# Performance work log

Hardware: AMD Instinct MI355X
Metric: run time of the kernel (lower is better)

The kernel has to match this reference:

```python
import jax, jax.numpy as jnp
import numpy as np

B, L, Z, H = 8, 256, 16, 256


def setup_inputs() -> dict:
    key = jax.random.key(0)
    k1, k2, k3, k4 = jax.random.split(key, 4)
    start_logits = jax.random.normal(k1, (B, L, H), dtype=jnp.float32)
    end_logits = jax.random.normal(k2, (B, L, H), dtype=jnp.float32)
    cls_logits = jax.random.normal(k3, (B, Z, H), dtype=jnp.float32)
    # nn.init.normal_(std=0.1)
    weight_start_end = 0.1 * jax.random.normal(k4, (H, H, H), dtype=jnp.float32)
    return {
        "start_logits": start_logits,
        "end_logits": end_logits,
        "cls_logits": cls_logits,
        "weight_start_end": weight_start_end,
    }


def reference(start_logits, end_logits, cls_logits, weight_start_end):
    # start: [b,x,i], weight: [i,o,j], end: [b,y,j], cls: [b,z,o]
    # Stage 1a: contract i ->  [b,x,o,j]  (GEMM: (b*x, i) @ (i, o*j))
    sw = jnp.einsum('bxi,ioj->bxoj', start_logits, weight_start_end)
    # Stage 1b: contract j ->  [b,x,y,o]
    start_end = jnp.einsum('bxoj,byj->bxyo', sw, end_logits)
    # Stage 2: contract o ->  [b,x,y,z]
    span_logits = jnp.einsum('bxyo,bzo->bxyz', start_end, cls_logits)
    return span_logits
```

## Files before the change

### kernel.cpp

```cpp
#include <hip/hip_runtime.h>


typedef __attribute__((ext_vector_type(8))) short          bf16x8;
typedef __attribute__((ext_vector_type(8))) unsigned short u16x8;
typedef __attribute__((ext_vector_type(4))) unsigned short u16x4;
typedef __attribute__((ext_vector_type(4))) float          f32x4;

#define LDST 40

__device__ __forceinline__ unsigned short f2bf(float f) {
    unsigned u = __builtin_bit_cast(unsigned, f);
    u += 0x7fff + ((u >> 16) & 1);
    return (unsigned short)(u >> 16);
}

template<bool AB16, bool BB16, bool T2OUT>
__global__ __launch_bounds__(512, 4)
void gemm_trans(const void* __restrict__ Abv, const void* __restrict__ Bbv,
                unsigned short* __restrict__ Cb,
                int lda, int ldb, int ldc,
                long aBS, int aSh, long bBS, long cBS)
{
    __shared__ unsigned short As[2][128 * LDST];
    __shared__ unsigned short Bs[2][128 * LDST];

    const int tid  = threadIdx.x;
    const int bz   = blockIdx.z;
    const int row0 = blockIdx.y * 128;
    const int col0 = blockIdx.x * 128;

    const float*          Af = (const float*)Abv          + (long)(bz >> aSh) * aBS;
    const unsigned short* Ah = (const unsigned short*)Abv + (long)(bz >> aSh) * aBS;
    const float*          Bf = (const float*)Bbv          + (long)bz * bBS;
    const unsigned short* Bh = (const unsigned short*)Bbv + (long)bz * bBS;

    const int ar  = tid >> 2;
    const int akc = tid & 3;
    const int kp  = (tid & 15) * 2;
    const int ng  = (tid >> 4) * 4;

    const int wid = tid >> 6, lane = tid & 63;
    const int wm = wid >> 1, wn = wid & 1;
    const int lr = lane & 15, lg = lane >> 4;

    f32x4 acc[2][4] = {};

    float4 aPf[2][2]; u16x8 aPh[2];
    float4 bPf[2][2]; u16x4 bPh[2][2];

    auto LOAD = [&](int set, int k0) {
        if constexpr (!AB16) {
            const float* p = Af + (long)(row0 + ar) * lda + k0 + akc * 8;
            aPf[set][0] = *(const float4*)p;
            aPf[set][1] = *(const float4*)(p + 4);
        } else {
            aPh[set] = *(const u16x8*)(Ah + (long)(row0 + ar) * lda + k0 + akc * 8);
        }
        if constexpr (!BB16) {
            const float* q = Bf + (long)(k0 + kp) * ldb + col0 + ng;
            bPf[set][0] = *(const float4*)q;
            bPf[set][1] = *(const float4*)(q + ldb);
        } else {
            const unsigned short* q = Bh + (long)(k0 + kp) * ldb + col0 + ng;
            bPh[set][0] = *(const u16x4*)q;
            bPh[set][1] = *(const u16x4*)(q + ldb);
        }
    };

    auto WRITE = [&](int set, int buf) {
        u16x8 w;
        if constexpr (!AB16) {
            const float* v = (const float*)&aPf[set][0];
#pragma unroll
            for (int e = 0; e < 8; ++e) w[e] = f2bf(v[e]);
        } else {
            w = aPh[set];
        }
        *(u16x8*)(As[buf] + ar * LDST + akc * 8) = w;

#pragma unroll
        for (int e = 0; e < 4; ++e) {
            unsigned lo, hi;
            if constexpr (!BB16) {
                const float* v0 = (const float*)&bPf[set][0];
                const float* v1 = (const float*)&bPf[set][1];
                lo = f2bf(v0[e]); hi = f2bf(v1[e]);
            } else {
                lo = bPh[set][0][e]; hi = bPh[set][1][e];
            }
            *(unsigned*)(Bs[buf] + (ng + e) * LDST + kp) = lo | (hi << 16);
        }
    };

    auto COMPUTE = [&](int buf) {
        bf16x8 aF[2], bF[4];
#pragma unroll
        for (int fm = 0; fm < 2; ++fm)
            aF[fm] = *(const bf16x8*)&As[buf][(wm * 32 + fm * 16 + lr) * LDST + lg * 8];
#pragma unroll
        for (int fn = 0; fn < 4; ++fn)
            bF[fn] = *(const bf16x8*)&Bs[buf][(wn * 64 + fn * 16 + lr) * LDST + lg * 8];
#pragma unroll
        for (int fm = 0; fm < 2; ++fm)
#pragma unroll
            for (int fn = 0; fn < 4; ++fn)
                acc[fm][fn] = __builtin_amdgcn_mfma_f32_16x16x32_bf16(
                    aF[fm], bF[fn], acc[fm][fn], 0, 0, 0);
    };

    LOAD(0, 0);
    WRITE(0, 0);
    LOAD(1, 32);
#pragma unroll
    for (int s = 0; s < 8; ++s) {
        asm volatile("s_waitcnt lgkmcnt(0)" ::: "memory");
        __builtin_amdgcn_s_barrier();
        if (s < 6) LOAD(s & 1, (s + 2) * 32);
        COMPUTE(s & 1);
        if (s < 7) WRITE((s + 1) & 1, (s + 1) & 1);
    }

#pragma unroll
    for (int fm = 0; fm < 2; ++fm)
#pragma unroll
        for (int q = 0; q < 4; ++q) {
            const long row = row0 + wm * 32 + fm * 16 + lg * 4 + q;
#pragma unroll
            for (int fn = 0; fn < 4; ++fn) {
                const int col = col0 + wn * 64 + fn * 16 + lr;
                if constexpr (T2OUT) {
                    unsigned short* Cq = Cb + (long)(bz >> 4) * 1048576 + (bz & 15) * 256;
                    Cq[row * 4096 + col] = f2bf(acc[fm][fn][q]);
                } else {
                    unsigned short* Cq = Cb + (long)bz * cBS;
                    Cq[row * (long)ldc + col] = f2bf(acc[fm][fn][q]);
                }
            }
        }
}

__global__ __launch_bounds__(256)
void fused_out(const unsigned short* __restrict__ endbf,
               const unsigned short* __restrict__ T2,
               float* __restrict__ out)
{
    const int tid = threadIdx.x;
    const int b  = blockIdx.x >> 7;
    const int xp = blockIdx.x & 127;
    const int wid = tid >> 6, lane = tid & 63;
    const int lr = lane & 15, lg = lane >> 4;

    const unsigned short* Arow = endbf + (long)b * 65536;
    const unsigned short* B0 = T2 + ((long)(b * 256 + xp * 2) * 16 + lr) * 256;
    const unsigned short* B1 = B0 + 4096;

    f32x4 acc0[4] = {}, acc1[4] = {};
    u16x8 a[2][4], pb0[2], pb1[2];

    auto LOADF = [&](int set, int k0) {
#pragma unroll
        for (int fm = 0; fm < 4; ++fm)
            a[set][fm] = *(const u16x8*)(Arow + (long)(wid * 64 + fm * 16 + lr) * 256 + k0 + lg * 8);
        pb0[set] = *(const u16x8*)(B0 + k0 + lg * 8);
        pb1[set] = *(const u16x8*)(B1 + k0 + lg * 8);
    };

    LOADF(0, 0);
#pragma unroll
    for (int s = 0; s < 8; ++s) {
        if (s < 7) LOADF((s + 1) & 1, (s + 1) * 32);
        __builtin_amdgcn_s_setprio(1);
#pragma unroll
        for (int fm = 0; fm < 4; ++fm) {
            acc0[fm] = __builtin_amdgcn_mfma_f32_16x16x32_bf16(
                __builtin_bit_cast(bf16x8, a[s & 1][fm]),
                __builtin_bit_cast(bf16x8, pb0[s & 1]), acc0[fm], 0, 0, 0);
            acc1[fm] = __builtin_amdgcn_mfma_f32_16x16x32_bf16(
                __builtin_bit_cast(bf16x8, a[s & 1][fm]),
                __builtin_bit_cast(bf16x8, pb1[s & 1]), acc1[fm], 0, 0, 0);
        }
        __builtin_amdgcn_s_setprio(0);
    }

    float* op0 = out + (long)(b * 256 + xp * 2) * 4096;
    float* op1 = op0 + 4096;
#pragma unroll
    for (int fm = 0; fm < 4; ++fm)
#pragma unroll
        for (int q = 0; q < 4; ++q) {
            const int y = wid * 64 + fm * 16 + lg * 4 + q;
            op0[y * 16 + lr] = acc0[fm][q];
            op1[y * 16 + lr] = acc1[fm][q];
        }
}

__global__ __launch_bounds__(256)
void cvt_bf16(const float* __restrict__ endl, const float* __restrict__ start,
              unsigned short* __restrict__ endbf, unsigned short* __restrict__ startbf)
{
    const int which = blockIdx.x >> 8;
    const float* in = which ? start : endl;
    unsigned short* out = which ? startbf : endbf;
    const int i = ((blockIdx.x & 255) * 256 + threadIdx.x) * 8;
    float4 v0 = *(const float4*)(in + i);
    float4 v1 = *(const float4*)(in + i + 4);
    const float* v = (const float*)&v0;
    u16x8 w;
#pragma unroll
    for (int e = 0; e < 4; ++e) w[e] = f2bf(v[e]);
    const float* u = (const float*)&v1;
#pragma unroll
    for (int e = 0; e < 4; ++e) w[4 + e] = f2bf(u[e]);
    *(u16x8*)(out + i) = w;
}

extern "C" void kernel_launch(void* const* d_in, const int* in_sizes, int n_in,
                              void* d_out, int out_size, void* d_ws, size_t ws_size,
                              hipStream_t stream)
{
    const float* start = (const float*)d_in[0];
    const float* endl  = (const float*)d_in[1];
    const float* cls   = (const float*)d_in[2];
    const float* W     = (const float*)d_in[3];
    float* out = (float*)d_out;

    char* ws = (char*)d_ws;
    unsigned short* Wc      = (unsigned short*)ws;
    unsigned short* T2      = (unsigned short*)(ws + 16777216);
    unsigned short* endbf   = (unsigned short*)(ws + 33554432);
    unsigned short* startbf = (unsigned short*)(ws + 34603008);

    hipLaunchKernelGGL(cvt_bf16, dim3(512), dim3(256), 0, stream,
        endl, start, endbf, startbf);

    hipLaunchKernelGGL((gemm_trans<false, false, false>), dim3(2, 1, 256), dim3(512), 0, stream,
        (const void*)cls, (const void*)W, Wc, 256, 256, 65536, 0L, 0, 65536L, 256L);

    hipLaunchKernelGGL((gemm_trans<true, true, true>), dim3(2, 2, 128), dim3(512), 0, stream,
        (const void*)startbf, (const void*)Wc, T2, 256, 256, 4096, 65536L, 4, 65536L, 0L);

    hipLaunchKernelGGL(fused_out, dim3(1024), dim3(256), 0, stream, endbf, T2, out);
}
```

Baseline: 158.6 us.

## Double GEMM K-tile to 64 and pre-convert cls to bf16

The transform GEMM now stages 64-wide K tiles instead of 32, with row padding raised to 72. Each thread issues wider 16-byte loads, the main loop runs 4 stages instead of 8, and MFMA bursts are wrapped in priority hints. This halves the barrier and synchronisation count per tile. The cls tensor is now converted to bf16 by the existing conversion kernel, so the first GEMM no longer converts fp32 A operands inline. The trade-off is that LDS use per block nearly doubles, which may reduce how many blocks fit on each CU.

```diff
diff --git a/kernel.cpp b/kernel.cpp
--- a/kernel.cpp
+++ b/kernel.cpp
@@ -3,10 +3,9 @@
 
 typedef __attribute__((ext_vector_type(8))) short          bf16x8;
 typedef __attribute__((ext_vector_type(8))) unsigned short u16x8;
-typedef __attribute__((ext_vector_type(4))) unsigned short u16x4;
 typedef __attribute__((ext_vector_type(4))) float          f32x4;
 
-#define LDST 40
+#define LDST 72
 
 __device__ __forceinline__ unsigned short f2bf(float f) {
     unsigned u = __builtin_bit_cast(unsigned, f);
@@ -14,9 +13,9 @@
     return (unsigned short)(u >> 16);
 }
 
-template<bool AB16, bool BB16, bool T2OUT>
+template<bool BB16, bool T2OUT>
 __global__ __launch_bounds__(512, 4)
-void gemm_trans(const void* __restrict__ Abv, const void* __restrict__ Bbv,
+void gemm_trans(const unsigned short* __restrict__ Ab, const void* __restrict__ Bbv,
                 unsigned short* __restrict__ Cb,
                 int lda, int ldb, int ldc,
                 long aBS, int aSh, long bBS, long cBS)
@@ -29,15 +28,14 @@
     const int row0 = blockIdx.y * 128;
     const int col0 = blockIdx.x * 128;
 
-    const float*          Af = (const float*)Abv          + (long)(bz >> aSh) * aBS;
-    const unsigned short* Ah = (const unsigned short*)Abv + (long)(bz >> aSh) * aBS;
+    const unsigned short* Ah = Ab + (long)(bz >> aSh) * aBS;
     const float*          Bf = (const float*)Bbv          + (long)bz * bBS;
     const unsigned short* Bh = (const unsigned short*)Bbv + (long)bz * bBS;
 
     const int ar  = tid >> 2;
-    const int akc = tid & 3;
-    const int kp  = (tid & 15) * 2;
-    const int ng  = (tid >> 4) * 4;
+    const int akc = (tid & 3) * 16;
+    const int kp  = (tid & 31) * 2;
+    const int ng  = (tid >> 5) * 8;
 
     const int wid = tid >> 6, lane = tid & 63;
     const int wm = wid >> 1, wn = wid & 1;
@@ -45,45 +43,36 @@
 
     f32x4 acc[2][4] = {};
 
-    float4 aPf[2][2]; u16x8 aPh[2];
-    float4 bPf[2][2]; u16x4 bPh[2][2];
+    u16x8  aP[2][2];
+    float4 bPf[2][4];
+    u16x8  bPh[2][2];
 
     auto LOAD = [&](int set, int k0) {
-        if constexpr (!AB16) {
-            const float* p = Af + (long)(row0 + ar) * lda + k0 + akc * 8;
-            aPf[set][0] = *(const float4*)p;
-            aPf[set][1] = *(const float4*)(p + 4);
-        } else {
-            aPh[set] = *(const u16x8*)(Ah + (long)(row0 + ar) * lda + k0 + akc * 8);
-        }
+        const unsigned short* p = Ah + (long)(row0 + ar) * lda + k0 + akc;
+        aP[set][0] = *(const u16x8*)p;
+        aP[set][1] = *(const u16x8*)(p + 8);
         if constexpr (!BB16) {
             const float* q = Bf + (long)(k0 + kp) * ldb + col0 + ng;
             bPf[set][0] = *(const float4*)q;
-            bPf[set][1] = *(const float4*)(q + ldb);
+            bPf[set][1] = *(const float4*)(q + 4);
+            bPf[set][2] = *(const float4*)(q + ldb);
+            bPf[set][3] = *(const float4*)(q + ldb + 4);
         } else {
             const unsigned short* q = Bh + (long)(k0 + kp) * ldb + col0 + ng;
-            bPh[set][0] = *(const u16x4*)q;
-            bPh[set][1] = *(const u16x4*)(q + ldb);
+            bPh[set][0] = *(const u16x8*)q;
+            bPh[set][1] = *(const u16x8*)(q + ldb);
         }
     };
 
     auto WRITE = [&](int set, int buf) {
-        u16x8 w;
-        if constexpr (!AB16) {
-            const float* v = (const float*)&aPf[set][0];
-#pragma unroll
-            for (int e = 0; e < 8; ++e) w[e] = f2bf(v[e]);
-        } else {
-            w = aPh[set];
-        }
-        *(u16x8*)(As[buf] + ar * LDST + akc * 8) = w;
-
-#pragma unroll
-        for (int e = 0; e < 4; ++e) {
+        *(u16x8*)(As[buf] + ar * LDST + akc)     = aP[set][0];
+        *(u16x8*)(As[buf] + ar * LDST + akc + 8) = aP[set][1];
+#pragma unroll
+        for (int e = 0; e < 8; ++e) {
             unsigned lo, hi;
             if constexpr (!BB16) {
                 const float* v0 = (const float*)&bPf[set][0];
-                const float* v1 = (const float*)&bPf[set][1];
+                const float* v1 = (const float*)&bPf[set][2];
                 lo = f2bf(v0[e]); hi = f2bf(v1[e]);
             } else {
                 lo = bPh[set][0][e]; hi = bPh[set][1][e];
@@ -93,31 +82,36 @@
     };
 
     auto COMPUTE = [&](int buf) {
-        bf16x8 aF[2], bF[4];
-#pragma unroll
-        for (int fm = 0; fm < 2; ++fm)
-            aF[fm] = *(const bf16x8*)&As[buf][(wm * 32 + fm * 16 + lr) * LDST + lg * 8];
-#pragma unroll
-        for (int fn = 0; fn < 4; ++fn)
-            bF[fn] = *(const bf16x8*)&Bs[buf][(wn * 64 + fn * 16 + lr) * LDST + lg * 8];
-#pragma unroll
-        for (int fm = 0; fm < 2; ++fm)
+#pragma unroll
+        for (int kk = 0; kk < 2; ++kk) {
+            bf16x8 aF[2], bF[4];
+#pragma unroll
+            for (int fm = 0; fm < 2; ++fm)
+                aF[fm] = *(const bf16x8*)&As[buf][(wm * 32 + fm * 16 + lr) * LDST + kk * 32 + lg * 8];
 #pragma unroll
             for (int fn = 0; fn < 4; ++fn)
-                acc[fm][fn] = __builtin_amdgcn_mfma_f32_16x16x32_bf16(
-                    aF[fm], bF[fn], acc[fm][fn], 0, 0, 0);
+                bF[fn] = *(const bf16x8*)&Bs[buf][(wn * 64 + fn * 16 + lr) * LDST + kk * 32 + lg * 8];
+            __builtin_amdgcn_s_setprio(1);
+#pragma unroll
+            for (int fm = 0; fm < 2; ++fm)
+#pragma unroll
+                for (int fn = 0; fn < 4; ++fn)
+                    acc[fm][fn] = __builtin_amdgcn_mfma_f32_16x16x32_bf16(
+                        aF[fm], bF[fn], acc[fm][fn], 0, 0, 0);
+            __builtin_amdgcn_s_setprio(0);
+        }
     };
 
     LOAD(0, 0);
     WRITE(0, 0);
-    LOAD(1, 32);
-#pragma unroll
-    for (int s = 0; s < 8; ++s) {
+    LOAD(1, 64);
+#pragma unroll
+    for (int s = 0; s < 4; ++s) {
         asm volatile("s_waitcnt lgkmcnt(0)" ::: "memory");
         __builtin_amdgcn_s_barrier();
-        if (s < 6) LOAD(s & 1, (s + 2) * 32);
+        if (s < 2) LOAD(s & 1, (s + 2) * 64);
         COMPUTE(s & 1);
-        if (s < 7) WRITE((s + 1) & 1, (s + 1) & 1);
+        if (s < 3) WRITE((s + 1) & 1, (s + 1) & 1);
     }
 
 #pragma unroll
@@ -196,11 +190,13 @@
 
 __global__ __launch_bounds__(256)
 void cvt_bf16(const float* __restrict__ endl, const float* __restrict__ start,
-              unsigned short* __restrict__ endbf, unsigned short* __restrict__ startbf)
+              const float* __restrict__ cls,
+              unsigned short* __restrict__ endbf, unsigned short* __restrict__ startbf,
+              unsigned short* __restrict__ clsbf)
 {
     const int which = blockIdx.x >> 8;
-    const float* in = which ? start : endl;
-    unsigned short* out = which ? startbf : endbf;
+    const float* in = which == 0 ? endl : (which == 1 ? start : cls);
+    unsigned short* out = which == 0 ? endbf : (which == 1 ? startbf : clsbf);
     const int i = ((blockIdx.x & 255) * 256 + threadIdx.x) * 8;
     float4 v0 = *(const float4*)(in + i);
     float4 v1 = *(const float4*)(in + i + 4);
@@ -229,15 +225,16 @@
     unsigned short* T2      = (unsigned short*)(ws + 16777216);
     unsigned short* endbf   = (unsigned short*)(ws + 33554432);
     unsigned short* startbf = (unsigned short*)(ws + 34603008);
-
-    hipLaunchKernelGGL(cvt_bf16, dim3(512), dim3(256), 0, stream,
-        endl, start, endbf, startbf);
-
-    hipLaunchKernelGGL((gemm_trans<false, false, false>), dim3(2, 1, 256), dim3(512), 0, stream,
-        (const void*)cls, (const void*)W, Wc, 256, 256, 65536, 0L, 0, 65536L, 256L);
-
-    hipLaunchKernelGGL((gemm_trans<true, true, true>), dim3(2, 2, 128), dim3(512), 0, stream,
-        (const void*)startbf, (const void*)Wc, T2, 256, 256, 4096, 65536L, 4, 65536L, 0L);
+    unsigned short* clsbf   = (unsigned short*)(ws + 35651584);
+
+    hipLaunchKernelGGL(cvt_bf16, dim3(528), dim3(256), 0, stream,
+        endl, start, cls, endbf, startbf, clsbf);
+
+    hipLaunchKernelGGL((gemm_trans<false, false>), dim3(2, 1, 256), dim3(512), 0, stream,
+        clsbf, (const void*)W, Wc, 256, 256, 65536, 0L, 0, 65536L, 256L);
+
+    hipLaunchKernelGGL((gemm_trans<true, true>), dim3(2, 2, 128), dim3(512), 0, stream,
+        startbf, (const void*)Wc, T2, 256, 256, 4096, 65536L, 4, 65536L, 0L);
 
     hipLaunchKernelGGL(fused_out, dim3(1024), dim3(256), 0, stream, endbf, T2, out);
 }
```

Result: faster. 155.1 us (-2.2%).
